# Performance work log

Measured on AMD Instinct MI355X. Metric: run time of the kernel, lower is better.

## Reference

```python
import jax, jax.numpy as jnp
import numpy as np

IN_F = 1024
OUT_F = 1024

def setup_inputs() -> dict:
    key = jax.random.key(0)
    ks = jax.random.split(key, 7)
    s = 1.0 / np.sqrt(IN_F)
    x = jax.random.normal(ks[0], (4, 2048, IN_F), dtype=jnp.float32)
    Wq = jax.random.uniform(ks[1], (OUT_F, IN_F), jnp.float32, -s, s)
    bq = jax.random.uniform(ks[2], (OUT_F,), jnp.float32, -s, s)
    Wk = jax.random.uniform(ks[3], (OUT_F, IN_F), jnp.float32, -s, s)
    bk = jax.random.uniform(ks[4], (OUT_F,), jnp.float32, -s, s)
    Wv = jax.random.uniform(ks[5], (OUT_F, IN_F), jnp.float32, -s, s)
    bv = jax.random.uniform(ks[6], (OUT_F,), jnp.float32, -s, s)
    return {"x": x, "Wq": Wq, "bq": bq, "Wk": Wk, "bk": bk, "Wv": Wv, "bv": bv}

def reference(x, Wq, bq, Wk, bk, Wv, bv):
    # Projector: ReLU(Linear(x))
    q = jax.nn.relu(jnp.einsum('bsd,od->bso', x, Wq) + bq)  # [B,S,O]
    k = jax.nn.relu(jnp.einsum('bsd,od->bso', x, Wk) + bk)
    v = jax.nn.relu(jnp.einsum('bsd,od->bso', x, Wv) + bv)
    logits = jnp.einsum('bio,bko->bik', q, k)  # unscaled QK^T, [B,S,S]
    scores = jax.nn.softmax(logits, axis=-1)
    out = jnp.einsum('bik,bko->bio', scores, v)
    return out
```

## Files before the change

kernel.cpp:

```cpp
#include <hip/hip_runtime.h>
#include <hip/hip_bf16.h>


#define SEQ 2048
#define DIM 1024
#define NB 4
#define MTOT (NB * SEQ)

typedef __attribute__((ext_vector_type(8))) short frag_ab;
typedef __attribute__((ext_vector_type(16))) float frag_c16;

__device__ __forceinline__ ushort f2bf(float f) {
    union { float f; unsigned u; } x; x.f = f;
    unsigned r = x.u + 0x7fffu + ((x.u >> 16) & 1u);
    return (ushort)(r >> 16);
}

typedef __attribute__((address_space(1))) const unsigned int guint;
typedef __attribute__((address_space(3))) unsigned int luint;

__device__ __forceinline__ void gld_lds16(const void* g, void* l) {
    __builtin_amdgcn_global_load_lds((guint*)g, (luint*)l, 16, 0, 0);
}

__device__ __forceinline__ void gemm_tiles(
    const ushort* __restrict__ A, size_t lda,
    const ushort* __restrict__ B, size_t ldb, int K,
    ushort* As, ushort* Bs, frag_c16 (&acc)[2][2])
{
    const int tid  = threadIdx.x;
    const int wave = tid >> 6;
    const int lane = tid & 63;
    const int l32  = lane & 31;
    const int half = lane >> 5;
    const int sr = wave * 16 + (lane >> 2);
    const int sc = lane & 3;
    const int wm = (wave & 1) * 64;
    const int wn = (wave >> 1) * 64;

    for (int k0 = 0; k0 < K; k0 += 32) {
        #pragma unroll
        for (int j = 0; j < 2; ++j) {
            int row = j * 64 + sr;
            int cg  = sc ^ ((row >> 1) & 3);
            ushort* la = As + (j * 64 + wave * 16) * 32;
            ushort* lb = Bs + (j * 64 + wave * 16) * 32;
            gld_lds16(A + (size_t)row * lda + k0 + cg * 8, la);
            gld_lds16(B + (size_t)row * ldb + k0 + cg * 8, lb);
        }
        __syncthreads();
        frag_ab af[2][2], bfr[2][2];
        #pragma unroll
        for (int mi = 0; mi < 2; ++mi) {
            int row = wm + mi * 32 + l32;
            int sw = (row >> 1) & 3;
            #pragma unroll
            for (int h = 0; h < 2; ++h) {
                int c = (h * 2 + half) ^ sw;
                af[mi][h] = *(const frag_ab*)&As[row * 32 + c * 8];
            }
        }
        #pragma unroll
        for (int ni = 0; ni < 2; ++ni) {
            int row = wn + ni * 32 + l32;
            int sw = (row >> 1) & 3;
            #pragma unroll
            for (int h = 0; h < 2; ++h) {
                int c = (h * 2 + half) ^ sw;
                bfr[ni][h] = *(const frag_ab*)&Bs[row * 32 + c * 8];
            }
        }
        #pragma unroll
        for (int h = 0; h < 2; ++h)
            #pragma unroll
            for (int mi = 0; mi < 2; ++mi)
                #pragma unroll
                for (int ni = 0; ni < 2; ++ni)
                    acc[mi][ni] = __builtin_amdgcn_mfma_f32_32x32x16_bf16(
                        af[mi][h], bfr[ni][h], acc[mi][ni], 0, 0, 0);
        __syncthreads();
    }
}


#define NX4 (MTOT * DIM / 4)
#define NW4 (DIM * DIM / 4)
__global__ __launch_bounds__(256) void cvt_kernel(
    const float* __restrict__ x,
    const float* __restrict__ Wq, const float* __restrict__ Wk,
    const float* __restrict__ Wv,
    ushort* __restrict__ xb, ushort* __restrict__ Wb)
{
    size_t i = (size_t)blockIdx.x * 256 + threadIdx.x;
    const float* src; ushort* dst; size_t idx;
    if (i < NX4) { src = x; dst = xb; idx = i; }
    else {
        size_t j = i - NX4;
        int w = (int)(j >> 18);
        idx = j & (NW4 - 1);
        src = w == 0 ? Wq : (w == 1 ? Wk : Wv);
        dst = Wb + (size_t)w * DIM * DIM;
    }
    float4 f = ((const float4*)src)[idx];
    ushort4 u; u.x = f2bf(f.x); u.y = f2bf(f.y); u.z = f2bf(f.z); u.w = f2bf(f.w);
    ((ushort4*)dst)[idx] = u;
}

__global__ __launch_bounds__(256) void qkproj_kernel(
    const ushort* __restrict__ xb, const ushort* __restrict__ Wb,
    const float* __restrict__ bq, const float* __restrict__ bk,
    ushort* __restrict__ q, ushort* __restrict__ k)
{
    const float* bias = blockIdx.z == 0 ? bq : bk;
    ushort* out       = blockIdx.z == 0 ? q  : k;
    const ushort* W = Wb + (size_t)blockIdx.z * DIM * DIM;

    __shared__ ushort As[128 * 32];
    __shared__ ushort Bs[128 * 32];

    const int tid  = threadIdx.x;
    const int wave = tid >> 6;
    const int lane = tid & 63;
    const int l32  = lane & 31;
    const int half = lane >> 5;
    const int m0 = blockIdx.x * 128;
    const int n0 = blockIdx.y * 128;
    const int wm = (wave & 1) * 64;
    const int wn = (wave >> 1) * 64;

    frag_c16 acc[2][2] = {};
    gemm_tiles(xb + (size_t)m0 * DIM, DIM, W + (size_t)n0 * DIM, DIM, DIM,
               As, Bs, acc);

    #pragma unroll
    for (int ni = 0; ni < 2; ++ni) {
        int col = n0 + wn + ni * 32 + l32;
        float bb = bias[col];
        #pragma unroll
        for (int mi = 0; mi < 2; ++mi)
            #pragma unroll
            for (int r = 0; r < 16; ++r) {
                int row = m0 + wm + mi * 32 + (r & 3) + 8 * (r >> 2) + 4 * half;
                float val = acc[mi][ni][r] + bb;
                val = val > 0.0f ? val : 0.0f;
                out[(size_t)row * DIM + col] = f2bf(val);
            }
    }
}

__global__ __launch_bounds__(256) void vproj_kernel(
    const ushort* __restrict__ xb, const ushort* __restrict__ Wv,
    const float* __restrict__ bv, ushort* __restrict__ vt)
{
    __shared__ ushort As[128 * 32];
    __shared__ ushort Bs[128 * 32];

    const int tid  = threadIdx.x;
    const int wave = tid >> 6;
    const int lane = tid & 63;
    const int l32  = lane & 31;
    const int half = lane >> 5;
    const int m0 = blockIdx.x * 128;
    const int n0 = blockIdx.y * 128;
    const int wm = (wave & 1) * 64;
    const int wn = (wave >> 1) * 64;

    frag_c16 acc[2][2] = {};
    gemm_tiles(xb + (size_t)m0 * DIM, DIM, Wv + (size_t)n0 * DIM, DIM, DIM,
               As, Bs, acc);

    const int bz = m0 >> 11;
    const int sb = (m0 & (SEQ - 1)) + wm;
    #pragma unroll
    for (int ni = 0; ni < 2; ++ni) {
        int col = n0 + wn + ni * 32 + l32;
        float bb = bv[col];
        ushort* vcol = vt + ((size_t)bz * DIM + col) * SEQ;
        #pragma unroll
        for (int mi = 0; mi < 2; ++mi)
            #pragma unroll
            for (int g = 0; g < 4; ++g) {
                int s0 = sb + mi * 32 + 8 * g + 4 * half;
                ushort4 u;
                float v0 = acc[mi][ni][4 * g + 0] + bb;
                float v1 = acc[mi][ni][4 * g + 1] + bb;
                float v2 = acc[mi][ni][4 * g + 2] + bb;
                float v3 = acc[mi][ni][4 * g + 3] + bb;
                u.x = f2bf(v0 > 0.0f ? v0 : 0.0f);
                u.y = f2bf(v1 > 0.0f ? v1 : 0.0f);
                u.z = f2bf(v2 > 0.0f ? v2 : 0.0f);
                u.w = f2bf(v3 > 0.0f ? v3 : 0.0f);
                *(ushort4*)&vcol[s0] = u;
            }
    }
}

__global__ __launch_bounds__(256) void qk_kernel(
    const ushort* __restrict__ q, const ushort* __restrict__ kk,
    float* __restrict__ logits)
{
    __shared__ ushort As[128 * 32];
    __shared__ ushort Bs[128 * 32];

    const int tid  = threadIdx.x;
    const int wave = tid >> 6;
    const int lane = tid & 63;
    const int l32  = lane & 31;
    const int half = lane >> 5;
    const int bz = blockIdx.z;
    const int m0 = blockIdx.x * 128;
    const int n0 = blockIdx.y * 128;
    const int wm = (wave & 1) * 64;
    const int wn = (wave >> 1) * 64;
    const size_t base = (size_t)bz * SEQ;

    frag_c16 acc[2][2] = {};
    gemm_tiles(q + (base + m0) * DIM, DIM, kk + (base + n0) * DIM, DIM, DIM,
               As, Bs, acc);

    #pragma unroll
    for (int mi = 0; mi < 2; ++mi)
        #pragma unroll
        for (int r = 0; r < 16; ++r) {
            int row = m0 + wm + mi * 32 + (r & 3) + 8 * (r >> 2) + 4 * half;
            #pragma unroll
            for (int ni = 0; ni < 2; ++ni) {
                int col = n0 + wn + ni * 32 + l32;
                logits[(base + row) * SEQ + col] = acc[mi][ni][r];
            }
        }
}

__global__ __launch_bounds__(256) void softmax_kernel(float* __restrict__ logits)
{
    float* p = logits + (size_t)blockIdx.x * SEQ;
    const int t = threadIdx.x;
    const int wave = t >> 6, lane = t & 63;

    float4 a = ((const float4*)p)[t];
    float4 b = ((const float4*)p)[t + 256];

    float m = fmaxf(fmaxf(fmaxf(a.x, a.y), fmaxf(a.z, a.w)),
                    fmaxf(fmaxf(b.x, b.y), fmaxf(b.z, b.w)));
    #pragma unroll
    for (int off = 32; off; off >>= 1) m = fmaxf(m, __shfl_down(m, off, 64));

    __shared__ float red[4];
    if (lane == 0) red[wave] = m;
    __syncthreads();
    m = fmaxf(fmaxf(red[0], red[1]), fmaxf(red[2], red[3]));

    a.x = __expf(a.x - m); a.y = __expf(a.y - m);
    a.z = __expf(a.z - m); a.w = __expf(a.w - m);
    b.x = __expf(b.x - m); b.y = __expf(b.y - m);
    b.z = __expf(b.z - m); b.w = __expf(b.w - m);

    float s = (a.x + a.y + a.z + a.w) + (b.x + b.y + b.z + b.w);
    #pragma unroll
    for (int off = 32; off; off >>= 1) s += __shfl_down(s, off, 64);
    __syncthreads();
    if (lane == 0) red[wave] = s;
    __syncthreads();
    s = red[0] + red[1] + red[2] + red[3];
    float inv = 1.0f / s;

    ushort* o = (ushort*)p;
    ushort4 u0, u1;
    u0.x = f2bf(a.x * inv); u0.y = f2bf(a.y * inv);
    u0.z = f2bf(a.z * inv); u0.w = f2bf(a.w * inv);
    u1.x = f2bf(b.x * inv); u1.y = f2bf(b.y * inv);
    u1.z = f2bf(b.z * inv); u1.w = f2bf(b.w * inv);
    ((ushort4*)o)[t]       = u0;
    ((ushort4*)o)[t + 256] = u1;
}

__global__ __launch_bounds__(256) void pv_kernel(
    const ushort* __restrict__ probs, const ushort* __restrict__ vt,
    float* __restrict__ out)
{
    __shared__ ushort As[128 * 32];
    __shared__ ushort Bs[128 * 32];

    const int tid  = threadIdx.x;
    const int wave = tid >> 6;
    const int lane = tid & 63;
    const int l32  = lane & 31;
    const int half = lane >> 5;
    const int bz = blockIdx.z;
    const int m0 = blockIdx.x * 128;
    const int n0 = blockIdx.y * 128;
    const int wm = (wave & 1) * 64;
    const int wn = (wave >> 1) * 64;

    frag_c16 acc[2][2] = {};
    gemm_tiles(probs + ((size_t)(bz * SEQ + m0)) * 4096, 4096,
               vt + ((size_t)(bz * DIM + n0)) * SEQ, SEQ, SEQ,
               As, Bs, acc);

    #pragma unroll
    for (int mi = 0; mi < 2; ++mi)
        #pragma unroll
        for (int r = 0; r < 16; ++r) {
            int row = m0 + wm + mi * 32 + (r & 3) + 8 * (r >> 2) + 4 * half;
            #pragma unroll
            for (int ni = 0; ni < 2; ++ni) {
                int col = n0 + wn + ni * 32 + l32;
                out[((size_t)(bz * SEQ + row)) * DIM + col] = acc[mi][ni][r];
            }
        }
}

extern "C" void kernel_launch(void* const* d_in, const int* in_sizes, int n_in,
                              void* d_out, int out_size, void* d_ws, size_t ws_size,
                              hipStream_t stream)
{
    const float* x  = (const float*)d_in[0];
    const float* Wq = (const float*)d_in[1];
    const float* bq = (const float*)d_in[2];
    const float* Wk = (const float*)d_in[3];
    const float* bk = (const float*)d_in[4];
    const float* Wv = (const float*)d_in[5];
    const float* bv = (const float*)d_in[6];
    float* out = (float*)d_out;

    char* ws = (char*)d_ws;
    ushort* q      = (ushort*)(ws);
    ushort* kk     = (ushort*)(ws + ((size_t)16 << 20));
    ushort* vt     = (ushort*)(ws + ((size_t)32 << 20));
    float*  logits = (float*) (ws + ((size_t)64 << 20));
    ushort* xb     = (ushort*)(ws + ((size_t)64 << 20));
    ushort* Wb     = (ushort*)(ws + ((size_t)80 << 20));

    cvt_kernel<<<dim3((NX4 + 3 * NW4) / 256), 256, 0, stream>>>(
        x, Wq, Wk, Wv, xb, Wb);

    qkproj_kernel<<<dim3(MTOT / 128, DIM / 128, 2), 256, 0, stream>>>(
        xb, Wb, bq, bk, q, kk);
    vproj_kernel<<<dim3(MTOT / 128, DIM / 128), 256, 0, stream>>>(
        xb, Wb + (size_t)2 * DIM * DIM, bv, vt);
    qk_kernel<<<dim3(SEQ / 128, SEQ / 128, NB), 256, 0, stream>>>(q, kk, logits);
    softmax_kernel<<<NB * SEQ, 256, 0, stream>>>(logits);
    pv_kernel<<<dim3(SEQ / 128, DIM / 128, NB), 256, 0, stream>>>(
        (const ushort*)logits, vt, out);
}
```

Measured before the change: 283.8 us.

## Shrink GEMM N-tile to 64 and add XCD-aware block swizzle for attention GEMMs

Halves the GEMM output tile width from 128 to 64 columns across all projection and attention GEMMs, doubling grid size so more blocks can be resident and the CUs are better filled. The QK and PV kernels also switch to a flat 1D grid, remapped so that blocks landing on the same XCD share a range of N-tiles, which is meant to improve L2 reuse of the B operand. The narrower tile lowers arithmetic intensity per block and adds more A-tile reloads from memory.

```diff
diff --git a/kernel.cpp b/kernel.cpp
--- a/kernel.cpp
+++ b/kernel.cpp
@@ -23,10 +23,10 @@
     __builtin_amdgcn_global_load_lds((guint*)g, (luint*)l, 16, 0, 0);
 }
 
-__device__ __forceinline__ void gemm_tiles(
+__device__ __forceinline__ void gemm_tiles_n64(
     const ushort* __restrict__ A, size_t lda,
     const ushort* __restrict__ B, size_t ldb, int K,
-    ushort* As, ushort* Bs, frag_c16 (&acc)[2][2])
+    ushort* As, ushort* Bs, frag_c16 (&acc)[2])
 {
     const int tid  = threadIdx.x;
     const int wave = tid >> 6;
@@ -36,20 +36,23 @@
     const int sr = wave * 16 + (lane >> 2);
     const int sc = lane & 3;
     const int wm = (wave & 1) * 64;
-    const int wn = (wave >> 1) * 64;
+    const int wn = (wave >> 1) * 32;
 
     for (int k0 = 0; k0 < K; k0 += 32) {
         #pragma unroll
         for (int j = 0; j < 2; ++j) {
             int row = j * 64 + sr;
             int cg  = sc ^ ((row >> 1) & 3);
-            ushort* la = As + (j * 64 + wave * 16) * 32;
-            ushort* lb = Bs + (j * 64 + wave * 16) * 32;
-            gld_lds16(A + (size_t)row * lda + k0 + cg * 8, la);
-            gld_lds16(B + (size_t)row * ldb + k0 + cg * 8, lb);
+            gld_lds16(A + (size_t)row * lda + k0 + cg * 8,
+                      As + (j * 64 + wave * 16) * 32);
+        }
+        {
+            int cg = sc ^ ((sr >> 1) & 3);
+            gld_lds16(B + (size_t)sr * ldb + k0 + cg * 8,
+                      Bs + (wave * 16) * 32);
         }
         __syncthreads();
-        frag_ab af[2][2], bfr[2][2];
+        frag_ab af[2][2], bf[2];
         #pragma unroll
         for (int mi = 0; mi < 2; ++mi) {
             int row = wm + mi * 32 + l32;
@@ -60,24 +63,21 @@
                 af[mi][h] = *(const frag_ab*)&As[row * 32 + c * 8];
             }
         }
-        #pragma unroll
-        for (int ni = 0; ni < 2; ++ni) {
-            int row = wn + ni * 32 + l32;
+        {
+            int row = wn + l32;
             int sw = (row >> 1) & 3;
             #pragma unroll
             for (int h = 0; h < 2; ++h) {
                 int c = (h * 2 + half) ^ sw;
-                bfr[ni][h] = *(const frag_ab*)&Bs[row * 32 + c * 8];
+                bf[h] = *(const frag_ab*)&Bs[row * 32 + c * 8];
             }
         }
         #pragma unroll
         for (int h = 0; h < 2; ++h)
             #pragma unroll
             for (int mi = 0; mi < 2; ++mi)
-                #pragma unroll
-                for (int ni = 0; ni < 2; ++ni)
-                    acc[mi][ni] = __builtin_amdgcn_mfma_f32_32x32x16_bf16(
-                        af[mi][h], bfr[ni][h], acc[mi][ni], 0, 0, 0);
+                acc[mi] = __builtin_amdgcn_mfma_f32_32x32x16_bf16(
+                    af[mi][h], bf[h], acc[mi], 0, 0, 0);
         __syncthreads();
     }
 }
@@ -116,7 +116,7 @@
     const ushort* W = Wb + (size_t)blockIdx.z * DIM * DIM;
 
     __shared__ ushort As[128 * 32];
-    __shared__ ushort Bs[128 * 32];
+    __shared__ ushort Bs[64 * 32];
 
     const int tid  = threadIdx.x;
     const int wave = tid >> 6;
@@ -124,28 +124,25 @@
     const int l32  = lane & 31;
     const int half = lane >> 5;
     const int m0 = blockIdx.x * 128;
-    const int n0 = blockIdx.y * 128;
-    const int wm = (wave & 1) * 64;
-    const int wn = (wave >> 1) * 64;
-
-    frag_c16 acc[2][2] = {};
-    gemm_tiles(xb + (size_t)m0 * DIM, DIM, W + (size_t)n0 * DIM, DIM, DIM,
-               As, Bs, acc);
-
-    #pragma unroll
-    for (int ni = 0; ni < 2; ++ni) {
-        int col = n0 + wn + ni * 32 + l32;
-        float bb = bias[col];
-        #pragma unroll
-        for (int mi = 0; mi < 2; ++mi)
-            #pragma unroll
-            for (int r = 0; r < 16; ++r) {
-                int row = m0 + wm + mi * 32 + (r & 3) + 8 * (r >> 2) + 4 * half;
-                float val = acc[mi][ni][r] + bb;
-                val = val > 0.0f ? val : 0.0f;
-                out[(size_t)row * DIM + col] = f2bf(val);
-            }
-    }
+    const int n0 = blockIdx.y * 64;
+    const int wm = (wave & 1) * 64;
+    const int wn = (wave >> 1) * 32;
+
+    frag_c16 acc[2] = {};
+    gemm_tiles_n64(xb + (size_t)m0 * DIM, DIM, W + (size_t)n0 * DIM, DIM, DIM,
+                   As, Bs, acc);
+
+    int col = n0 + wn + l32;
+    float bb = bias[col];
+    #pragma unroll
+    for (int mi = 0; mi < 2; ++mi)
+        #pragma unroll
+        for (int r = 0; r < 16; ++r) {
+            int row = m0 + wm + mi * 32 + (r & 3) + 8 * (r >> 2) + 4 * half;
+            float val = acc[mi][r] + bb;
+            val = val > 0.0f ? val : 0.0f;
+            out[(size_t)row * DIM + col] = f2bf(val);
+        }
 }
 
 __global__ __launch_bounds__(256) void vproj_kernel(
@@ -153,7 +150,7 @@
     const float* __restrict__ bv, ushort* __restrict__ vt)
 {
     __shared__ ushort As[128 * 32];
-    __shared__ ushort Bs[128 * 32];
+    __shared__ ushort Bs[64 * 32];
 
     const int tid  = threadIdx.x;
     const int wave = tid >> 6;
@@ -161,38 +158,35 @@
     const int l32  = lane & 31;
     const int half = lane >> 5;
     const int m0 = blockIdx.x * 128;
-    const int n0 = blockIdx.y * 128;
-    const int wm = (wave & 1) * 64;
-    const int wn = (wave >> 1) * 64;
-
-    frag_c16 acc[2][2] = {};
-    gemm_tiles(xb + (size_t)m0 * DIM, DIM, Wv + (size_t)n0 * DIM, DIM, DIM,
-               As, Bs, acc);
+    const int n0 = blockIdx.y * 64;
+    const int wm = (wave & 1) * 64;
+    const int wn = (wave >> 1) * 32;
+
+    frag_c16 acc[2] = {};
+    gemm_tiles_n64(xb + (size_t)m0 * DIM, DIM, Wv + (size_t)n0 * DIM, DIM, DIM,
+                   As, Bs, acc);
 
     const int bz = m0 >> 11;
     const int sb = (m0 & (SEQ - 1)) + wm;
-    #pragma unroll
-    for (int ni = 0; ni < 2; ++ni) {
-        int col = n0 + wn + ni * 32 + l32;
-        float bb = bv[col];
-        ushort* vcol = vt + ((size_t)bz * DIM + col) * SEQ;
-        #pragma unroll
-        for (int mi = 0; mi < 2; ++mi)
-            #pragma unroll
-            for (int g = 0; g < 4; ++g) {
-                int s0 = sb + mi * 32 + 8 * g + 4 * half;
-                ushort4 u;
-                float v0 = acc[mi][ni][4 * g + 0] + bb;
-                float v1 = acc[mi][ni][4 * g + 1] + bb;
-                float v2 = acc[mi][ni][4 * g + 2] + bb;
-                float v3 = acc[mi][ni][4 * g + 3] + bb;
-                u.x = f2bf(v0 > 0.0f ? v0 : 0.0f);
-                u.y = f2bf(v1 > 0.0f ? v1 : 0.0f);
-                u.z = f2bf(v2 > 0.0f ? v2 : 0.0f);
-                u.w = f2bf(v3 > 0.0f ? v3 : 0.0f);
-                *(ushort4*)&vcol[s0] = u;
-            }
-    }
+    int col = n0 + wn + l32;
+    float bb = bv[col];
+    ushort* vcol = vt + ((size_t)bz * DIM + col) * SEQ;
+    #pragma unroll
+    for (int mi = 0; mi < 2; ++mi)
+        #pragma unroll
+        for (int g = 0; g < 4; ++g) {
+            int s0 = sb + mi * 32 + 8 * g + 4 * half;
+            ushort4 u;
+            float v0 = acc[mi][4 * g + 0] + bb;
+            float v1 = acc[mi][4 * g + 1] + bb;
+            float v2 = acc[mi][4 * g + 2] + bb;
+            float v3 = acc[mi][4 * g + 3] + bb;
+            u.x = f2bf(v0 > 0.0f ? v0 : 0.0f);
+            u.y = f2bf(v1 > 0.0f ? v1 : 0.0f);
+            u.z = f2bf(v2 > 0.0f ? v2 : 0.0f);
+            u.w = f2bf(v3 > 0.0f ? v3 : 0.0f);
+            *(ushort4*)&vcol[s0] = u;
+        }
 }
 
 __global__ __launch_bounds__(256) void qk_kernel(
@@ -200,34 +194,38 @@
     float* __restrict__ logits)
 {
     __shared__ ushort As[128 * 32];
-    __shared__ ushort Bs[128 * 32];
-
-    const int tid  = threadIdx.x;
-    const int wave = tid >> 6;
-    const int lane = tid & 63;
-    const int l32  = lane & 31;
-    const int half = lane >> 5;
-    const int bz = blockIdx.z;
-    const int m0 = blockIdx.x * 128;
-    const int n0 = blockIdx.y * 128;
-    const int wm = (wave & 1) * 64;
-    const int wn = (wave >> 1) * 64;
+    __shared__ ushort Bs[64 * 32];
+
+    const int bid = blockIdx.x;
+    const int xcd = bid & 7;
+    const int idx = bid >> 3;
+    const int bz  = idx >> 6;
+    const int t   = idx & 63;
+    const int nt  = xcd * 4 + (t & 3);
+    const int mt  = t >> 2;
+
+    const int tid  = threadIdx.x;
+    const int wave = tid >> 6;
+    const int lane = tid & 63;
+    const int l32  = lane & 31;
+    const int half = lane >> 5;
+    const int m0 = mt * 128;
+    const int n0 = nt * 64;
+    const int wm = (wave & 1) * 64;
+    const int wn = (wave >> 1) * 32;
     const size_t base = (size_t)bz * SEQ;
 
-    frag_c16 acc[2][2] = {};
-    gemm_tiles(q + (base + m0) * DIM, DIM, kk + (base + n0) * DIM, DIM, DIM,
-               As, Bs, acc);
-
+    frag_c16 acc[2] = {};
+    gemm_tiles_n64(q + (base + m0) * DIM, DIM, kk + (base + n0) * DIM, DIM, DIM,
+                   As, Bs, acc);
+
+    int col = n0 + wn + l32;
     #pragma unroll
     for (int mi = 0; mi < 2; ++mi)
         #pragma unroll
         for (int r = 0; r < 16; ++r) {
             int row = m0 + wm + mi * 32 + (r & 3) + 8 * (r >> 2) + 4 * half;
-            #pragma unroll
-            for (int ni = 0; ni < 2; ++ni) {
-                int col = n0 + wn + ni * 32 + l32;
-                logits[(base + row) * SEQ + col] = acc[mi][ni][r];
-            }
+            logits[(base + row) * SEQ + col] = acc[mi][r];
         }
 }
 
@@ -279,34 +277,38 @@
     float* __restrict__ out)
 {
     __shared__ ushort As[128 * 32];
-    __shared__ ushort Bs[128 * 32];
-
-    const int tid  = threadIdx.x;
-    const int wave = tid >> 6;
-    const int lane = tid & 63;
-    const int l32  = lane & 31;
-    const int half = lane >> 5;
-    const int bz = blockIdx.z;
-    const int m0 = blockIdx.x * 128;
-    const int n0 = blockIdx.y * 128;
-    const int wm = (wave & 1) * 64;
-    const int wn = (wave >> 1) * 64;
-
-    frag_c16 acc[2][2] = {};
-    gemm_tiles(probs + ((size_t)(bz * SEQ + m0)) * 4096, 4096,
-               vt + ((size_t)(bz * DIM + n0)) * SEQ, SEQ, SEQ,
-               As, Bs, acc);
-
+    __shared__ ushort Bs[64 * 32];
+
+    const int bid = blockIdx.x;
+    const int xcd = bid & 7;
+    const int idx = bid >> 3;
+    const int bz  = idx >> 5;
+    const int t   = idx & 31;
+    const int nt  = xcd * 2 + (t & 1);
+    const int mt  = t >> 1;
+
+    const int tid  = threadIdx.x;
+    const int wave = tid >> 6;
+    const int lane = tid & 63;
+    const int l32  = lane & 31;
+    const int half = lane >> 5;
+    const int m0 = mt * 128;
+    const int n0 = nt * 64;
+    const int wm = (wave & 1) * 64;
+    const int wn = (wave >> 1) * 32;
+
+    frag_c16 acc[2] = {};
+    gemm_tiles_n64(probs + ((size_t)(bz * SEQ + m0)) * 4096, 4096,
+                   vt + ((size_t)(bz * DIM + n0)) * SEQ, SEQ, SEQ,
+                   As, Bs, acc);
+
+    int col = n0 + wn + l32;
     #pragma unroll
     for (int mi = 0; mi < 2; ++mi)
         #pragma unroll
         for (int r = 0; r < 16; ++r) {
             int row = m0 + wm + mi * 32 + (r & 3) + 8 * (r >> 2) + 4 * half;
-            #pragma unroll
-            for (int ni = 0; ni < 2; ++ni) {
-                int col = n0 + wn + ni * 32 + l32;
-                out[((size_t)(bz * SEQ + row)) * DIM + col] = acc[mi][ni][r];
-            }
+            out[((size_t)(bz * SEQ + row)) * DIM + col] = acc[mi][r];
         }
 }
 
@@ -334,12 +336,12 @@
     cvt_kernel<<<dim3((NX4 + 3 * NW4) / 256), 256, 0, stream>>>(
         x, Wq, Wk, Wv, xb, Wb);
 
-    qkproj_kernel<<<dim3(MTOT / 128, DIM / 128, 2), 256, 0, stream>>>(
+    qkproj_kernel<<<dim3(MTOT / 128, DIM / 64, 2), 256, 0, stream>>>(
         xb, Wb, bq, bk, q, kk);
-    vproj_kernel<<<dim3(MTOT / 128, DIM / 128), 256, 0, stream>>>(
+    vproj_kernel<<<dim3(MTOT / 128, DIM / 64), 256, 0, stream>>>(
         xb, Wb + (size_t)2 * DIM * DIM, bv, vt);
-    qk_kernel<<<dim3(SEQ / 128, SEQ / 128, NB), 256, 0, stream>>>(q, kk, logits);
+    qk_kernel<<<dim3(2048), 256, 0, stream>>>(q, kk, logits);
     softmax_kernel<<<NB * SEQ, 256, 0, stream>>>(logits);
-    pv_kernel<<<dim3(SEQ / 128, DIM / 128, NB), 256, 0, stream>>>(
+    pv_kernel<<<dim3(1024), 256, 0, stream>>>(
         (const ushort*)logits, vt, out);
 }
```

Measured after the change: 314.8 us. 10.9% more time.
